# Kernel optimization log

Hardware: AMD Instinct MI355X
Metric: run time of the kernel (lower is better)

## Reference

```python
import math
import jax, jax.numpy as jnp
import numpy as np

B, T, D, L, E = 2, 1024, 1024, 12, 4
EPS = 1e-5


def _ln(v, g, b):
    mu = jnp.mean(v, axis=-1, keepdims=True)
    var = jnp.mean(jnp.square(v - mu), axis=-1, keepdims=True)
    return (v - mu) * jax.lax.rsqrt(var + EPS) * g + b


def setup_inputs() -> dict:
    key = jax.random.key(0)
    ks = jax.random.split(key, 4)
    x = jax.random.normal(ks[0], (B, T, D), dtype=jnp.float32)
    queries = jax.random.normal(ks[1], (L, D), dtype=jnp.float32) * 0.02
    W1 = jax.random.normal(ks[2], (L, D, E * D), dtype=jnp.float32) * 0.02
    W2 = jax.random.normal(ks[3], (L, E * D, D), dtype=jnp.float32) * 0.02
    return {
        'x': x,
        'queries': queries,
        'kn_g': jnp.ones((L, D), jnp.float32),
        'kn_b': jnp.zeros((L, D), jnp.float32),
        'ln_g': jnp.ones((L, D), jnp.float32),
        'ln_b': jnp.zeros((L, D), jnp.float32),
        'W1': W1,
        'b1': jnp.zeros((L, E * D), jnp.float32),
        'W2': W2,
        'b2': jnp.zeros((L, D), jnp.float32),
    }


def reference(x, queries, kn_g, kn_b, ln_g, ln_b, W1, b1, W2, b2):
    scale = 1.0 / math.sqrt(D)
    history = [x]
    h = x
    for l in range(L):
        V = jnp.stack(history, axis=0)              # (l+1, B, T, D)
        K = _ln(V, kn_g[l], kn_b[l])
        scores = jnp.einsum('d,lbtd->lbt', queries[l], K) * scale
        alpha = jax.nn.softmax(scores, axis=0)       # softmax over history axis
        residual = jnp.einsum('lbt,lbtd->btd', alpha, V)
        u = _ln(h, ln_g[l], ln_b[l])
        ff = jax.nn.gelu(u @ W1[l] + b1[l], approximate=False) @ W2[l] + b2[l]
        h = residual + ff
        history.append(h)
    return h
```

## Files before the change

### kernel.cpp

```cpp
#include <hip/hip_runtime.h>
#include <math.h>

#define BATCH 2
#define TSEQ 1024
#define DIM 1024
#define NLAYER 12
#define EDIM 4096
#define BT 2048
#define EPS_LN 1e-5f

typedef __attribute__((ext_vector_type(4))) float  f32x4;
typedef __attribute__((ext_vector_type(8))) __bf16 bf16x8;
typedef __attribute__((ext_vector_type(4))) __bf16 bf16x4;

__device__ __forceinline__ void gl_lds16(const void* gptr, void* lptr) {
    __builtin_amdgcn_global_load_lds(
        (const __attribute__((address_space(1))) void*)gptr,
        (__attribute__((address_space(3))) void*)lptr,
        16, 0, 0);
}

__device__ __forceinline__ void wtile256(float (*t)[65], const float* src,
                                         __bf16* dst, int R, int C,
                                         int rt, int ct, int tid)
{
    int lr = tid >> 2, cs = (tid & 3) << 4;
    const float* sp = src + (size_t)(rt * 64 + lr) * C + ct * 64 + cs;
#pragma unroll
    for (int s = 0; s < 4; s++) {
        f32x4 v = *(const f32x4*)(sp + s * 4);
        t[lr][cs + s * 4 + 0] = v[0];
        t[lr][cs + s * 4 + 1] = v[1];
        t[lr][cs + s * 4 + 2] = v[2];
        t[lr][cs + s * 4 + 3] = v[3];
    }
    __syncthreads();
    int oc = tid >> 2, rs = (tid & 3) << 4;
    bf16x8 o0, o1;
#pragma unroll
    for (int e = 0; e < 8; e++) o0[e] = (__bf16)t[rs + e][oc];
#pragma unroll
    for (int e = 0; e < 8; e++) o1[e] = (__bf16)t[rs + 8 + e][oc];
    __bf16* dp = dst + (size_t)(ct * 64 + oc) * R + rt * 64 + rs;
    *(bf16x8*)dp = o0;
    *(bf16x8*)(dp + 8) = o1;
}

__global__ __launch_bounds__(256) void wtrans_kernel(
    const float* __restrict__ W1, const float* __restrict__ W2,
    __bf16* __restrict__ W1t, __bf16* __restrict__ W2t)
{
    __shared__ float t[64][65];
    int z = blockIdx.z;
    if (z == 0) wtile256(t, W1, W1t, DIM, EDIM, blockIdx.y, blockIdx.x, threadIdx.x);
    else        wtile256(t, W2, W2t, EDIM, DIM, blockIdx.x, blockIdx.y, threadIdx.x);
}

__global__ __launch_bounds__(256)
void attn_wt_kernel(const float* __restrict__ x,
                    const float* __restrict__ hist,
                    const __bf16* __restrict__ part,
                    const float* __restrict__ q,
                    const float* __restrict__ kng,
                    const float* __restrict__ knb,
                    const float* __restrict__ lng,
                    const float* __restrict__ lnb,
                    const float* __restrict__ b2,
                    float* __restrict__ hnext,
                    __bf16* __restrict__ u,
                    int nl,
                    const float* __restrict__ W1n,
                    const float* __restrict__ W2n,
                    __bf16* __restrict__ W1tn,
                    __bf16* __restrict__ W2tn,
                    int dowt)
{
    __shared__ char smem[49408];

    if (blockIdx.x >= BT) {
        if (!dowt) return;
        float (*t)[65] = (float(*)[65])smem;
        int tile = blockIdx.x - BT;
        if (tile < 1024) wtile256(t, W1n, W1tn, DIM, EDIM, tile >> 6, tile & 63, threadIdx.x);
        else { int t3 = tile - 1024; wtile256(t, W2n, W2tn, EDIM, DIM, t3 & 63, t3 >> 6, threadIdx.x); }
        return;
    }

    float (*V)[DIM] = (float(*)[DIM])smem;
    float* sS  = (float*)(smem + 49152);
    float* sMu = sS + NLAYER;
    float* sRs = sMu + NLAYER;

    const int bt = blockIdx.x;
    const int tid = threadIdx.x, lane = tid & 63, w = tid >> 6;

    f32x4 gqv[4];
    float sg = 0.f, sb = 0.f;
#pragma unroll
    for (int i = 0; i < 4; i++) {
        int d = i * 256 + lane * 4;
        f32x4 g4 = *(const f32x4*)(kng + d);
        f32x4 q4 = *(const f32x4*)(q + d);
        f32x4 b4 = *(const f32x4*)(knb + d);
#pragma unroll
        for (int c = 0; c < 4; c++) {
            float gq = g4[c] * q4[c];
            gqv[i][c] = gq;
            sg += gq;
            sb += b4[c] * q4[c];
        }
    }
#pragma unroll
    for (int off = 32; off; off >>= 1) {
        sg += __shfl_xor(sg, off);
        sb += __shfl_xor(sb, off);
    }

    for (int lp = w; lp < nl; lp += 4) {
        const float* vp = (lp == 0) ? (x + (size_t)bt * DIM)
                                    : (hist + ((size_t)(lp - 1) * BT + bt) * DIM);
        f32x4 vv[4];
#pragma unroll
        for (int i = 0; i < 4; i++) vv[i] = *(const f32x4*)(vp + i * 256 + lane * 4);

        if (part && lp == nl - 1) {
#pragma unroll
            for (int z = 0; z < 4; z++) {
                const __bf16* pp = part + ((size_t)z * BT + bt) * DIM;
#pragma unroll
                for (int i = 0; i < 4; i++) {
                    bf16x4 p4 = *(const bf16x4*)(pp + i * 256 + lane * 4);
#pragma unroll
                    for (int c = 0; c < 4; c++) vv[i][c] += (float)p4[c];
                }
            }
            float* wb = const_cast<float*>(vp);
#pragma unroll
            for (int i = 0; i < 4; i++) *(f32x4*)(wb + i * 256 + lane * 4) = vv[i];
        }

        float s1 = 0.f, s2 = 0.f, sq = 0.f;
#pragma unroll
        for (int i = 0; i < 4; i++) {
            *(f32x4*)(&V[lp][i * 256 + lane * 4]) = vv[i];
#pragma unroll
            for (int c = 0; c < 4; c++) {
                float xv = vv[i][c];
                s1 += xv; s2 += xv * xv; sq += xv * gqv[i][c];
            }
        }
#pragma unroll
        for (int off = 32; off; off >>= 1) {
            s1 += __shfl_xor(s1, off);
            s2 += __shfl_xor(s2, off);
            sq += __shfl_xor(sq, off);
        }
        if (lane == 0) {
            float mu = s1 * (1.0f / DIM);
            float var = s2 * (1.0f / DIM) - mu * mu;
            float rs = rsqrtf(var + EPS_LN);
            sMu[lp] = mu; sRs[lp] = rs;
            sS[lp] = (rs * (sq - mu * sg) + sb) * (1.0f / 32.0f);
        }
    }
    __syncthreads();

    float mx = -1e30f;
#pragma unroll
    for (int i = 0; i < NLAYER; i++) if (i < nl) mx = fmaxf(mx, sS[i]);
    float al[NLAYER];
    float ssum = 0.f;
#pragma unroll
    for (int i = 0; i < NLAYER; i++) {
        al[i] = (i < nl) ? __expf(sS[i] - mx) : 0.f;
        ssum += al[i];
    }
    float inv = 1.0f / ssum;

    const int d = tid * 4;
    f32x4 r; r[0] = 0.f; r[1] = 0.f; r[2] = 0.f; r[3] = 0.f;
#pragma unroll
    for (int i = 0; i < NLAYER; i++) {
        if (i < nl) {
            f32x4 v4 = *(const f32x4*)(&V[i][d]);
            float a = al[i] * inv;
            r[0] += a * v4[0]; r[1] += a * v4[1]; r[2] += a * v4[2]; r[3] += a * v4[3];
        }
    }
    f32x4 h4 = *(const f32x4*)(&V[nl - 1][d]);
    f32x4 b24 = *(const f32x4*)(b2 + d);
    f32x4 ro; ro[0] = r[0] + b24[0]; ro[1] = r[1] + b24[1];
    ro[2] = r[2] + b24[2]; ro[3] = r[3] + b24[3];
    *(f32x4*)(hnext + (size_t)bt * DIM + d) = ro;

    float mu = sMu[nl - 1], rs = sRs[nl - 1];
    f32x4 g4 = *(const f32x4*)(lng + d);
    f32x4 b4 = *(const f32x4*)(lnb + d);
    bf16x4 uo;
#pragma unroll
    for (int c = 0; c < 4; c++) uo[c] = (__bf16)((h4[c] - mu) * rs * g4[c] + b4[c]);
    *(bf16x4*)(u + (size_t)bt * DIM + d) = uo;
}

#define STG 49152

template <int EPI>
__global__ __launch_bounds__(512, 1)
void gemm8(const __bf16* __restrict__ A, const __bf16* __restrict__ Bt,
           const float* __restrict__ bias, void* __restrict__ outp,
           int N, int As, int Bs)
{
    __shared__ char lds[3 * STG];
    const int tid = threadIdx.x, lane = tid & 63, w = tid >> 6;
    const int wm = w >> 2, wn = w & 3;
    const int lr = lane & 15;
    const int hib = (lane >> 4) << 4;
    const int NT = 16;

    const int nb = gridDim.x;
    const int fid = blockIdx.x;
    const int swz = (fid & 7) * (nb >> 3) + (fid >> 3);
    const int m0 = (swz & 15) * 128;
    const int n0 = (swz >> 4) * 256;
    const int kbase = blockIdx.y * 1024;

    f32x4 acc[4][4];
#pragma unroll
    for (int i = 0; i < 4; i++)
#pragma unroll
        for (int j = 0; j < 4; j++) { acc[i][j][0]=0.f; acc[i][j][1]=0.f; acc[i][j][2]=0.f; acc[i][j][3]=0.f; }

    const int srow = tid >> 3;
    const int ksrc = ((tid & 7) << 4) ^ ((srow & 7) << 4);
    const char* Ac = (const char*)A;
    const char* Bc = (const char*)Bt;
    size_t aoff[2], boff[4];
#pragma unroll
    for (int c = 0; c < 2; c++)
        aoff[c] = ((size_t)(m0 + c * 64 + srow) * As + kbase) * 2 + ksrc;
#pragma unroll
    for (int c = 0; c < 4; c++)
        boff[c] = ((size_t)(n0 + c * 64 + srow) * Bs + kbase) * 2 + ksrc;

    char* abw = lds + w * 1024;
    char* bbw = lds + 16384 + w * 1024;

    auto STAGE = [&](int tt, int bi) {
        size_t kb = (size_t)tt * 128;
        char* ab = abw + bi * STG;
        char* bb = bbw + bi * STG;
#pragma unroll
        for (int c = 0; c < 2; c++) gl_lds16(Ac + aoff[c] + kb, ab + c * 8192);
#pragma unroll
        for (int c = 0; c < 4; c++) gl_lds16(Bc + boff[c] + kb, bb + c * 8192);
    };

    STAGE(0, 0);
    STAGE(1, 1);

    int sb = 0, st = 2;
#pragma unroll 1
    for (int t = 0; t < NT; ++t) {
        if (t < NT - 1) asm volatile("s_waitcnt vmcnt(6)" ::: "memory");
        else            asm volatile("s_waitcnt vmcnt(0)" ::: "memory");
        __builtin_amdgcn_s_barrier();
        __builtin_amdgcn_sched_barrier(0);

        if (t + 2 < NT) STAGE(t + 2, st);

        const char* base = lds + sb * STG;
        bf16x8 af[2][4], bfr[2][4];
#pragma unroll
        for (int kk = 0; kk < 2; kk++) {
#pragma unroll
            for (int i = 0; i < 4; i++) {
                int ra = wm * 64 + i * 16 + lr;
                af[kk][i] = *(const bf16x8*)(base + ra * 128 + ((kk * 64 + hib) ^ ((ra & 7) << 4)));
            }
#pragma unroll
            for (int j = 0; j < 4; j++) {
                int rb = wn * 64 + j * 16 + lr;
                bfr[kk][j] = *(const bf16x8*)(base + 16384 + rb * 128 + ((kk * 64 + hib) ^ ((rb & 7) << 4)));
            }
        }
        __builtin_amdgcn_s_setprio(1);
#pragma unroll
        for (int kk = 0; kk < 2; kk++)
#pragma unroll
            for (int i = 0; i < 4; i++)
#pragma unroll
                for (int j = 0; j < 4; j++)
                    acc[i][j] = __builtin_amdgcn_mfma_f32_16x16x32_bf16(af[kk][i], bfr[kk][j], acc[i][j], 0, 0, 0);
        __builtin_amdgcn_s_setprio(0);

        sb = (sb == 2) ? 0 : sb + 1;
        st = (st == 2) ? 0 : st + 1;
    }

    const int lrow = (lane >> 4) << 2;
    if (EPI == 0) {
        __bf16* out = (__bf16*)outp;
#pragma unroll
        for (int i = 0; i < 4; i++) {
#pragma unroll
            for (int j = 0; j < 4; j++) {
                int colg = n0 + wn * 64 + j * 16 + lr;
                float bc = bias[colg];
#pragma unroll
                for (int r = 0; r < 4; r++) {
                    int rowg = m0 + wm * 64 + i * 16 + lrow + r;
                    float v = acc[i][j][r] + bc;
                    float tt2 = 0.7978845608f * (v + 0.044715f * v * v * v);
                    float e = __expf(2.0f * tt2);
                    float th = 1.0f - 2.0f / (e + 1.0f);
                    out[(size_t)rowg * N + colg] = (__bf16)(0.5f * v * (1.0f + th));
                }
            }
        }
    } else {
        __bf16* out = (__bf16*)outp + (size_t)blockIdx.y * BT * N;
#pragma unroll
        for (int i = 0; i < 4; i++) {
#pragma unroll
            for (int j = 0; j < 4; j++) {
                int colg = n0 + wn * 64 + j * 16 + lr;
#pragma unroll
                for (int r = 0; r < 4; r++) {
                    int rowg = m0 + wm * 64 + i * 16 + lrow + r;
                    out[(size_t)rowg * N + colg] = (__bf16)acc[i][j][r];
                }
            }
        }
    }
}

__global__ void final_reduce(const float* __restrict__ base,
                             const __bf16* __restrict__ part,
                             float* __restrict__ out)
{
    size_t i = ((size_t)blockIdx.x * 256 + threadIdx.x) * 4;
    f32x4 r = *(const f32x4*)(base + i);
#pragma unroll
    for (int z = 0; z < 4; z++) {
        bf16x4 p = *(const bf16x4*)(part + (size_t)z * BT * DIM + i);
#pragma unroll
        for (int c = 0; c < 4; c++) r[c] += (float)p[c];
    }
    *(f32x4*)(out + i) = r;
}

extern "C" void kernel_launch(void* const* d_in, const int* in_sizes, int n_in,
                              void* d_out, int out_size, void* d_ws, size_t ws_size,
                              hipStream_t stream)
{
    const float* x   = (const float*)d_in[0];
    const float* q   = (const float*)d_in[1];
    const float* kng = (const float*)d_in[2];
    const float* knb = (const float*)d_in[3];
    const float* lng = (const float*)d_in[4];
    const float* lnb = (const float*)d_in[5];
    const float* W1  = (const float*)d_in[6];
    const float* b1  = (const float*)d_in[7];
    const float* W2  = (const float*)d_in[8];
    const float* b2  = (const float*)d_in[9];

    char* ws = (char*)d_ws;
    const size_t slot = (size_t)BT * DIM;
    float*  hist  = (float*)(ws);
    __bf16* ubuf  = (__bf16*)(ws + 100663296);
    __bf16* hmid  = (__bf16*)(ws + 104857600);
    __bf16* W1tb[2] = { (__bf16*)(ws + 121634816), (__bf16*)(ws + 130023424) };
    __bf16* W2tb[2] = { (__bf16*)(ws + 138412032), (__bf16*)(ws + 146800640) };
    __bf16* part  = (__bf16*)(ws + 155189248);

    wtrans_kernel<<<dim3(64, 16, 2), 256, 0, stream>>>(W1, W2, W1tb[0], W2tb[0]);

    for (int l = 0; l < NLAYER; l++) {
        int nl = l + 1;
        int ln = (l + 1 < NLAYER) ? l + 1 : l;
        float* hnext = hist + (size_t)l * slot;
        attn_wt_kernel<<<dim3(2 * BT), 256, 0, stream>>>(
            x, hist, (l >= 1) ? part : (const __bf16*)nullptr,
            q + (size_t)l * DIM,
            kng + (size_t)l * DIM, knb + (size_t)l * DIM,
            lng + (size_t)l * DIM, lnb + (size_t)l * DIM,
            b2 + (size_t)l * DIM, hnext, ubuf, nl,
            W1 + (size_t)ln * DIM * EDIM, W2 + (size_t)ln * EDIM * DIM,
            W1tb[(l + 1) & 1], W2tb[(l + 1) & 1], (l + 1 < NLAYER) ? 1 : 0);
        gemm8<0><<<dim3(256, 1), 512, 0, stream>>>(
            ubuf, W1tb[l & 1], b1 + (size_t)l * EDIM, (void*)hmid, EDIM, DIM, DIM);
        gemm8<2><<<dim3(64, 4), 512, 0, stream>>>(
            hmid, W2tb[l & 1], nullptr, (void*)part, DIM, EDIM, EDIM);
    }

    final_reduce<<<dim3(BT * DIM / 1024), 256, 0, stream>>>(
        hist + (size_t)(NLAYER - 1) * slot, part, (float*)d_out);
}
```

Measured before the change: 916.2 us.

## Store layer history in bf16 and drop GEMM block swizzle

Keeps earlier history entries as bf16 in a separate buffer. Only the newest layer's base is kept in fp32, in two ping-pong buffers. This roughly halves the history bytes the attention kernel reads every layer, with reduced precision on older history values in the depth-attention mix. It also removes the block-index swizzle in the GEMM kernel and uses direct m/n tile mapping, which may change L2 locality.

```diff
diff --git a/kernel.cpp b/kernel.cpp
--- a/kernel.cpp
+++ b/kernel.cpp
@@ -58,7 +58,8 @@
 
 __global__ __launch_bounds__(256)
 void attn_wt_kernel(const float* __restrict__ x,
-                    const float* __restrict__ hist,
+                    const float* __restrict__ baseprev,
+                    __bf16* __restrict__ histbf,
                     const __bf16* __restrict__ part,
                     const float* __restrict__ q,
                     const float* __restrict__ kng,
@@ -117,26 +118,42 @@
     }
 
     for (int lp = w; lp < nl; lp += 4) {
-        const float* vp = (lp == 0) ? (x + (size_t)bt * DIM)
-                                    : (hist + ((size_t)(lp - 1) * BT + bt) * DIM);
         f32x4 vv[4];
-#pragma unroll
-        for (int i = 0; i < 4; i++) vv[i] = *(const f32x4*)(vp + i * 256 + lane * 4);
-
-        if (part && lp == nl - 1) {
-#pragma unroll
-            for (int z = 0; z < 4; z++) {
-                const __bf16* pp = part + ((size_t)z * BT + bt) * DIM;
+        if (lp == nl - 1) {
+            const float* vp = (nl == 1) ? (x + (size_t)bt * DIM)
+                                        : (baseprev + (size_t)bt * DIM);
+#pragma unroll
+            for (int i = 0; i < 4; i++) vv[i] = *(const f32x4*)(vp + i * 256 + lane * 4);
+            if (part) {
+#pragma unroll
+                for (int z = 0; z < 4; z++) {
+                    const __bf16* pp = part + ((size_t)z * BT + bt) * DIM;
+#pragma unroll
+                    for (int i = 0; i < 4; i++) {
+                        bf16x4 p4 = *(const bf16x4*)(pp + i * 256 + lane * 4);
+#pragma unroll
+                        for (int c = 0; c < 4; c++) vv[i][c] += (float)p4[c];
+                    }
+                }
+            }
+            if (nl < NLAYER) {
+                __bf16* mp = histbf + ((size_t)lp * BT + bt) * DIM;
 #pragma unroll
                 for (int i = 0; i < 4; i++) {
-                    bf16x4 p4 = *(const bf16x4*)(pp + i * 256 + lane * 4);
-#pragma unroll
-                    for (int c = 0; c < 4; c++) vv[i][c] += (float)p4[c];
+                    bf16x4 m4;
+#pragma unroll
+                    for (int c = 0; c < 4; c++) m4[c] = (__bf16)vv[i][c];
+                    *(bf16x4*)(mp + i * 256 + lane * 4) = m4;
                 }
             }
-            float* wb = const_cast<float*>(vp);
-#pragma unroll
-            for (int i = 0; i < 4; i++) *(f32x4*)(wb + i * 256 + lane * 4) = vv[i];
+        } else {
+            const __bf16* mp = histbf + ((size_t)lp * BT + bt) * DIM;
+#pragma unroll
+            for (int i = 0; i < 4; i++) {
+                bf16x4 m4 = *(const bf16x4*)(mp + i * 256 + lane * 4);
+#pragma unroll
+                for (int c = 0; c < 4; c++) vv[i][c] = (float)m4[c];
+            }
         }
 
         float s1 = 0.f, s2 = 0.f, sq = 0.f;
@@ -217,11 +234,9 @@
     const int hib = (lane >> 4) << 4;
     const int NT = 16;
 
-    const int nb = gridDim.x;
     const int fid = blockIdx.x;
-    const int swz = (fid & 7) * (nb >> 3) + (fid >> 3);
-    const int m0 = (swz & 15) * 128;
-    const int n0 = (swz >> 4) * 256;
+    const int m0 = (fid & 15) * 128;
+    const int n0 = (fid >> 4) * 256;
     const int kbase = blockIdx.y * 1024;
 
     f32x4 acc[4][4];
@@ -365,22 +380,24 @@
     const float* b2  = (const float*)d_in[9];
 
     char* ws = (char*)d_ws;
-    const size_t slot = (size_t)BT * DIM;
-    float*  hist  = (float*)(ws);
-    __bf16* ubuf  = (__bf16*)(ws + 100663296);
-    __bf16* hmid  = (__bf16*)(ws + 104857600);
-    __bf16* W1tb[2] = { (__bf16*)(ws + 121634816), (__bf16*)(ws + 130023424) };
-    __bf16* W2tb[2] = { (__bf16*)(ws + 138412032), (__bf16*)(ws + 146800640) };
-    __bf16* part  = (__bf16*)(ws + 155189248);
+    const size_t MB = 1048576;
+    float*  base2[2] = { (float*)(ws), (float*)(ws + 8 * MB) };
+    __bf16* histbf = (__bf16*)(ws + 16 * MB);
+    __bf16* ubuf   = (__bf16*)(ws + 64 * MB);
+    __bf16* hmid   = (__bf16*)(ws + 68 * MB);
+    __bf16* W1tb[2] = { (__bf16*)(ws + 84 * MB), (__bf16*)(ws + 92 * MB) };
+    __bf16* W2tb[2] = { (__bf16*)(ws + 100 * MB), (__bf16*)(ws + 108 * MB) };
+    __bf16* part   = (__bf16*)(ws + 116 * MB);
 
     wtrans_kernel<<<dim3(64, 16, 2), 256, 0, stream>>>(W1, W2, W1tb[0], W2tb[0]);
 
     for (int l = 0; l < NLAYER; l++) {
         int nl = l + 1;
         int ln = (l + 1 < NLAYER) ? l + 1 : l;
-        float* hnext = hist + (size_t)l * slot;
+        float* hnext = base2[l & 1];
+        const float* bprev = base2[(l + 1) & 1];
         attn_wt_kernel<<<dim3(2 * BT), 256, 0, stream>>>(
-            x, hist, (l >= 1) ? part : (const __bf16*)nullptr,
+            x, bprev, histbf, (l >= 1) ? part : (const __bf16*)nullptr,
             q + (size_t)l * DIM,
             kng + (size_t)l * DIM, knb + (size_t)l * DIM,
             lng + (size_t)l * DIM, lnb + (size_t)l * DIM,
@@ -394,5 +411,5 @@
     }
 
     final_reduce<<<dim3(BT * DIM / 1024), 256, 0, stream>>>(
-        hist + (size_t)(NLAYER - 1) * slot, part, (float*)d_out);
-}
+        base2[1], part, (float*)d_out);
+}
```

Measured after the change: 897.0 us. 1.02x faster.
